# Performance work log

Hardware: AMD Instinct MI355X
Metric: run time of the kernel (lower is better)

Reference implementation:

```python
import jax, jax.numpy as jnp
import numpy as np

V = 256       # num_variables
D = 512       # hidden_dim
B = 1024      # batch


def setup_inputs() -> dict:
    key = jax.random.key(0)
    ks = jax.random.split(key, 8)
    s1 = 1.0 / np.sqrt(V + 1)
    s2 = 1.0 / np.sqrt(D)
    return {
        "x": jax.random.normal(ks[0], (B, V), dtype=jnp.float32),
        "adjacency": jax.random.normal(ks[1], (V, V), dtype=jnp.float32),
        "W1": jax.random.normal(ks[2], (V, D, V + 1), dtype=jnp.float32) * s1,
        "b1": jax.random.normal(ks[3], (V, D), dtype=jnp.float32) * s1,
        "W2": jax.random.normal(ks[4], (V, D, D), dtype=jnp.float32) * s2,
        "b2": jax.random.normal(ks[5], (V, D), dtype=jnp.float32) * s2,
        "W3": jax.random.normal(ks[6], (V, D), dtype=jnp.float32) * s2,
        "b3": jax.random.normal(ks[7], (V,), dtype=jnp.float32) * s2,
    }


def reference(x, adjacency, W1, b1, W2, b2, W3, b3):
    # weighted_x[b, i] = (x @ A.T)[b, i]
    wx = x @ adjacency.T  # [B, V]
    # combined input for variable i: cat([x, wx[:, i:i+1]]) -> width V+1
    # build [B, V, V+1] by broadcasting x across the variable axis
    x_b = jnp.broadcast_to(x[:, None, :], (x.shape[0], V, V))
    comb = jnp.concatenate([x_b, wx[:, :, None]], axis=-1)  # [B, V, V+1]
    # per-variable 3-layer MLP, batched over the variable axis i
    h1 = jax.nn.relu(jnp.einsum('bij,idj->bid', comb, W1) + b1)   # [B, V, D]
    h2 = jax.nn.relu(jnp.einsum('bid,ied->bie', h1, W2) + b2)     # [B, V, D]
    out = jnp.einsum('bid,id->bi', h2, W3) + b3                   # [B, V]
    return out
```

## Files before the change

kernel.cpp:

```cpp
#include <hip/hip_runtime.h>
#include <hip/hip_bf16.h>
#include <stdint.h>

#define VNUM 256
#define DNUM 512
#define BNUM 1024

typedef __attribute__((ext_vector_type(8))) short bf16x8;
typedef __attribute__((ext_vector_type(4))) float f32x4;

__device__ __forceinline__ uint16_t f2bf(float f) {
    uint32_t u = __float_as_uint(f);
    uint32_t r = (u + 0x7FFFu + ((u >> 16) & 1u)) >> 16;
    return (uint16_t)r;
}

__device__ __forceinline__ void gl_lds16(const void* g, void* l) {
    __builtin_amdgcn_global_load_lds(
        (const __attribute__((address_space(1))) uint32_t*)g,
        (__attribute__((address_space(3))) uint32_t*)l, 16, 0, 0);
}

__global__ __launch_bounds__(256) void wx_kernel(const float* __restrict__ x,
                                                 const float* __restrict__ adj,
                                                 float* __restrict__ wx) {
    __shared__ float xs[64][36];
    __shared__ float as_[64][36];
    const int b0 = blockIdx.x * 64, i0 = blockIdx.y * 64;
    const int t = threadIdx.x;
    const int tx = t & 15, ty = t >> 4;
    const int lr = t >> 2, lk = (t & 3) * 8;
    float c[4][4] = {};
    for (int k0 = 0; k0 < 256; k0 += 32) {
        __syncthreads();
        *(float4*)&xs[lr][lk]      = *(const float4*)&x[(size_t)(b0 + lr) * VNUM + k0 + lk];
        *(float4*)&xs[lr][lk + 4]  = *(const float4*)&x[(size_t)(b0 + lr) * VNUM + k0 + lk + 4];
        *(float4*)&as_[lr][lk]     = *(const float4*)&adj[(size_t)(i0 + lr) * VNUM + k0 + lk];
        *(float4*)&as_[lr][lk + 4] = *(const float4*)&adj[(size_t)(i0 + lr) * VNUM + k0 + lk + 4];
        __syncthreads();
        #pragma unroll
        for (int kk = 0; kk < 32; kk++) {
            float xv[4], av[4];
            #pragma unroll
            for (int a = 0; a < 4; a++) xv[a] = xs[ty + a * 16][kk];
            #pragma unroll
            for (int b = 0; b < 4; b++) av[b] = as_[tx + b * 16][kk];
            #pragma unroll
            for (int a = 0; a < 4; a++)
                #pragma unroll
                for (int b = 0; b < 4; b++) c[a][b] += xv[a] * av[b];
        }
    }
    #pragma unroll
    for (int a = 0; a < 4; a++)
        #pragma unroll
        for (int b = 0; b < 4; b++)
            wx[(size_t)(b0 + ty + a * 16) * VNUM + i0 + tx + b * 16] = c[a][b];
}

__global__ __launch_bounds__(256) void xcvt_kernel(const float* __restrict__ x,
                                                   uint16_t* __restrict__ xbf) {
    const int idx = (blockIdx.x * 256 + threadIdx.x) * 4;
    float4 v = *(const float4*)&x[idx];
    uint32_t p0 = (uint32_t)f2bf(v.x) | ((uint32_t)f2bf(v.y) << 16);
    uint32_t p1 = (uint32_t)f2bf(v.z) | ((uint32_t)f2bf(v.w) << 16);
    *(uint2*)&xbf[idx] = make_uint2(p0, p1);
}

__global__ __launch_bounds__(256) void gemm1_kernel(const uint16_t* __restrict__ xbf,
                                                    const float* __restrict__ wx,
                                                    const float* __restrict__ W1,
                                                    const float* __restrict__ b1,
                                                    uint16_t* __restrict__ h1,
                                                    int ivar_base) {
    const int b0 = blockIdx.x * 128;
    const int d0 = blockIdx.y * 128;
    const int ci = blockIdx.z;
    const int i  = ivar_base + ci;

    __shared__ __align__(16) uint16_t As[128 * 32];
    __shared__ __align__(16) uint16_t Bs[128 * 32];
    __shared__ float wxs[128], w1ls[128], b1s[128];

    const int t = threadIdx.x;
    const int w = t >> 6, l = t & 63;
    const int wm = w >> 1, wn = w & 1;
    const int q = l >> 4, lo = l & 15;

    if (t < 128) {
        wxs[t] = wx[(size_t)(b0 + t) * VNUM + i];
        b1s[t] = b1[(size_t)i * DNUM + d0 + t];
    } else {
        int tt = t - 128;
        w1ls[tt] = W1[((size_t)i * DNUM + d0 + tt) * 257 + 256];
    }

    f32x4 acc[4][4];
    #pragma unroll
    for (int a = 0; a < 4; a++)
        #pragma unroll
        for (int b = 0; b < 4; b++) { f32x4 z = {0.f, 0.f, 0.f, 0.f}; acc[a][b] = z; }

    const int br = t >> 1, kh = t & 1;
    const float* bsrc_row = W1 + ((size_t)i * DNUM + d0 + br) * 257 + kh * 16;
    const int sB = (br >> 1) & 3;
    const int bslot0 = br * 32 + (((kh * 2 + 0) ^ sB) * 8);
    const int bslot1 = br * 32 + (((kh * 2 + 1) ^ sB) * 8);

    for (int k0 = 0; k0 < 256; k0 += 32) {
        __syncthreads();
        #pragma unroll
        for (int p = 0; p < 2; p++) {
            int c  = p * 256 + w * 64 + l;
            int r  = c >> 2, k2 = c & 3;
            int gk2 = k2 ^ ((r >> 1) & 3);
            gl_lds16(xbf + (size_t)(b0 + r) * VNUM + k0 + gk2 * 8,
                     &As[(p * 256 + w * 64) * 8]);
        }
        {
            const float* s = bsrc_row + k0;
            float f[16];
            #pragma unroll
            for (int j = 0; j < 16; j++) f[j] = s[j];
            uint32_t pk[8];
            #pragma unroll
            for (int j = 0; j < 8; j++)
                pk[j] = (uint32_t)f2bf(f[2 * j]) | ((uint32_t)f2bf(f[2 * j + 1]) << 16);
            *(uint4*)&Bs[bslot0] = make_uint4(pk[0], pk[1], pk[2], pk[3]);
            *(uint4*)&Bs[bslot1] = make_uint4(pk[4], pk[5], pk[6], pk[7]);
        }
        __syncthreads();
        bf16x8 af[4], bfr[4];
        #pragma unroll
        for (int mt = 0; mt < 4; mt++) {
            int m = wm * 64 + mt * 16 + lo;
            int slot = q ^ ((m >> 1) & 3);
            af[mt] = *(const bf16x8*)&As[m * 32 + slot * 8];
        }
        #pragma unroll
        for (int nt = 0; nt < 4; nt++) {
            int n = wn * 64 + nt * 16 + lo;
            int slot = q ^ ((n >> 1) & 3);
            bfr[nt] = *(const bf16x8*)&Bs[n * 32 + slot * 8];
        }
        #pragma unroll
        for (int mt = 0; mt < 4; mt++)
            #pragma unroll
            for (int nt = 0; nt < 4; nt++)
                acc[mt][nt] = __builtin_amdgcn_mfma_f32_16x16x32_bf16(af[mt], bfr[nt], acc[mt][nt], 0, 0, 0);
    }

    #pragma unroll
    for (int mt = 0; mt < 4; mt++) {
        #pragma unroll
        for (int reg = 0; reg < 4; reg++) {
            int row = wm * 64 + mt * 16 + q * 4 + reg;
            size_t rowbase = ((size_t)ci * BNUM + b0 + row) * DNUM + d0;
            float wxv = wxs[row];
            #pragma unroll
            for (int nt = 0; nt < 4; nt++) {
                int col = wn * 64 + nt * 16 + lo;
                float v = acc[mt][nt][reg] + wxv * w1ls[col] + b1s[col];
                v = fmaxf(v, 0.f);
                h1[rowbase + col] = f2bf(v);
            }
        }
    }
}

__global__ __launch_bounds__(256) void gemm2_kernel(const uint16_t* __restrict__ h1,
                                                    const float* __restrict__ W2,
                                                    const float* __restrict__ b2,
                                                    const float* __restrict__ W3,
                                                    const float* __restrict__ b3,
                                                    float* __restrict__ out,
                                                    int ivar_base) {
    const int b0 = blockIdx.x * 128;
    const int e0 = blockIdx.y * 128;
    const int ci = blockIdx.z;
    const int i  = ivar_base + ci;

    __shared__ __align__(16) uint16_t As[128 * 32];
    __shared__ __align__(16) uint16_t Bs[128 * 32];
    __shared__ float b2s[128], w3s[128];
    __shared__ float red[2][128];

    const int t = threadIdx.x;
    const int w = t >> 6, l = t & 63;
    const int wm = w >> 1, wn = w & 1;
    const int q = l >> 4, lo = l & 15;

    if (t < 128) b2s[t] = b2[(size_t)i * DNUM + e0 + t];
    else         w3s[t - 128] = W3[(size_t)i * DNUM + e0 + (t - 128)];

    f32x4 acc[4][4];
    #pragma unroll
    for (int a = 0; a < 4; a++)
        #pragma unroll
        for (int b = 0; b < 4; b++) { f32x4 z = {0.f, 0.f, 0.f, 0.f}; acc[a][b] = z; }

    const int br = t >> 1, kh = t & 1;
    const float* bsrc_row = W2 + ((size_t)i * DNUM + e0 + br) * DNUM + kh * 16;
    const int sB = (br >> 1) & 3;
    const int bslot0 = br * 32 + (((kh * 2 + 0) ^ sB) * 8);
    const int bslot1 = br * 32 + (((kh * 2 + 1) ^ sB) * 8);

    const uint16_t* abase = h1 + (size_t)ci * BNUM * DNUM;

    for (int k0 = 0; k0 < 512; k0 += 32) {
        __syncthreads();
        #pragma unroll
        for (int p = 0; p < 2; p++) {
            int c  = p * 256 + w * 64 + l;
            int r  = c >> 2, k2 = c & 3;
            int gk2 = k2 ^ ((r >> 1) & 3);
            gl_lds16(abase + (size_t)(b0 + r) * DNUM + k0 + gk2 * 8,
                     &As[(p * 256 + w * 64) * 8]);
        }
        {
            const float4* s = (const float4*)(bsrc_row + k0);
            float4 fa = s[0], fb = s[1], fc = s[2], fd = s[3];
            uint32_t p0 = (uint32_t)f2bf(fa.x) | ((uint32_t)f2bf(fa.y) << 16);
            uint32_t p1 = (uint32_t)f2bf(fa.z) | ((uint32_t)f2bf(fa.w) << 16);
            uint32_t p2 = (uint32_t)f2bf(fb.x) | ((uint32_t)f2bf(fb.y) << 16);
            uint32_t p3 = (uint32_t)f2bf(fb.z) | ((uint32_t)f2bf(fb.w) << 16);
            uint32_t p4 = (uint32_t)f2bf(fc.x) | ((uint32_t)f2bf(fc.y) << 16);
            uint32_t p5 = (uint32_t)f2bf(fc.z) | ((uint32_t)f2bf(fc.w) << 16);
            uint32_t p6 = (uint32_t)f2bf(fd.x) | ((uint32_t)f2bf(fd.y) << 16);
            uint32_t p7 = (uint32_t)f2bf(fd.z) | ((uint32_t)f2bf(fd.w) << 16);
            *(uint4*)&Bs[bslot0] = make_uint4(p0, p1, p2, p3);
            *(uint4*)&Bs[bslot1] = make_uint4(p4, p5, p6, p7);
        }
        __syncthreads();
        bf16x8 af[4], bfr[4];
        #pragma unroll
        for (int mt = 0; mt < 4; mt++) {
            int m = wm * 64 + mt * 16 + lo;
            int slot = q ^ ((m >> 1) & 3);
            af[mt] = *(const bf16x8*)&As[m * 32 + slot * 8];
        }
        #pragma unroll
        for (int nt = 0; nt < 4; nt++) {
            int n = wn * 64 + nt * 16 + lo;
            int slot = q ^ ((n >> 1) & 3);
            bfr[nt] = *(const bf16x8*)&Bs[n * 32 + slot * 8];
        }
        #pragma unroll
        for (int mt = 0; mt < 4; mt++)
            #pragma unroll
            for (int nt = 0; nt < 4; nt++)
                acc[mt][nt] = __builtin_amdgcn_mfma_f32_16x16x32_bf16(af[mt], bfr[nt], acc[mt][nt], 0, 0, 0);
    }

    float rs[4][4];
    #pragma unroll
    for (int mt = 0; mt < 4; mt++) {
        #pragma unroll
        for (int reg = 0; reg < 4; reg++) {
            float v = 0.f;
            #pragma unroll
            for (int nt = 0; nt < 4; nt++) {
                int col = wn * 64 + nt * 16 + lo;
                float h = acc[mt][nt][reg] + b2s[col];
                h = fmaxf(h, 0.f);
                v += h * w3s[col];
            }
            v += __shfl_xor(v, 1, 64);
            v += __shfl_xor(v, 2, 64);
            v += __shfl_xor(v, 4, 64);
            v += __shfl_xor(v, 8, 64);
            rs[mt][reg] = v;
        }
    }
    if (lo == 0) {
        #pragma unroll
        for (int mt = 0; mt < 4; mt++)
            #pragma unroll
            for (int reg = 0; reg < 4; reg++) {
                int row = wm * 64 + mt * 16 + q * 4 + reg;
                red[wn][row] = rs[mt][reg];
            }
    }
    __syncthreads();
    if (t < 128) {
        float v = red[0][t] + red[1][t];
        if (e0 == 0) v += b3[i];
        atomicAdd(&out[(size_t)(b0 + t) * VNUM + i], v);
    }
}

extern "C" void kernel_launch(void* const* d_in, const int* in_sizes, int n_in,
                              void* d_out, int out_size, void* d_ws, size_t ws_size,
                              hipStream_t stream) {
    const float* x   = (const float*)d_in[0];
    const float* adj = (const float*)d_in[1];
    const float* W1  = (const float*)d_in[2];
    const float* b1  = (const float*)d_in[3];
    const float* W2  = (const float*)d_in[4];
    const float* b2  = (const float*)d_in[5];
    const float* W3  = (const float*)d_in[6];
    const float* b3  = (const float*)d_in[7];
    float* out = (float*)d_out;

    char* ws = (char*)d_ws;
    float*    wx  = (float*)ws;
    uint16_t* xbf = (uint16_t*)(ws + (1 << 20));
    uint16_t* h1  = (uint16_t*)(ws + (1 << 20) + (1 << 19));

    const size_t fixed = (1 << 20) + (1 << 19);
    int CV = 64;
    while (CV > 1 && ws_size < fixed + (size_t)CV * BNUM * DNUM * 2) CV >>= 1;

    hipMemsetAsync(d_out, 0, (size_t)BNUM * VNUM * sizeof(float), stream);
    wx_kernel<<<dim3(16, 4), 256, 0, stream>>>(x, adj, wx);
    xcvt_kernel<<<256, 256, 0, stream>>>(x, xbf);
    for (int c = 0; c < VNUM; c += CV) {
        gemm1_kernel<<<dim3(8, 4, CV), 256, 0, stream>>>(xbf, wx, W1, b1, h1, c);
        gemm2_kernel<<<dim3(8, 4, CV), 256, 0, stream>>>(h1, W2, b2, W3, b3, out, c);
    }
}
```

Measured before the change: 1.007 ms.

## Pre-convert W1/W2 to bf16 and run all variables in one launch

Adds separate kernels that convert W1 (splitting off its last column) and W2 to bf16 up front, so both GEMMs stream B tiles straight into LDS with global_load_lds instead of loading fp32, converting and storing per tile. It also drops the chunked loop over variables and launches each GEMM once over all 256 variables, which needs h1 for every variable in the workspace (about 256 MB). The cost is an extra full fp32 read plus bf16 write of the weights each call, in exchange for halving the weight bytes each GEMM tile reads and removing conversion work from the inner loop. It assumes the workspace is large enough and no longer checks ws_size.

```diff
diff --git a/kernel.cpp b/kernel.cpp
--- a/kernel.cpp
+++ b/kernel.cpp
@@ -67,16 +67,36 @@
     *(uint2*)&xbf[idx] = make_uint2(p0, p1);
 }
 
+__global__ __launch_bounds__(256) void w1cvt_kernel(const float* __restrict__ W1,
+                                                    uint16_t* __restrict__ W1bf,
+                                                    float* __restrict__ w1last) {
+    const size_t idx = (size_t)blockIdx.x * 256 + threadIdx.x;
+    const size_t row = idx >> 8;
+    const int    k   = (int)(idx & 255);
+    const float* src = W1 + row * 257;
+    W1bf[idx] = f2bf(src[k]);
+    if (k == 0) w1last[row] = src[256];
+}
+
+__global__ __launch_bounds__(256) void w2cvt_kernel(const float* __restrict__ W2,
+                                                    uint16_t* __restrict__ W2bf) {
+    const size_t idx = ((size_t)blockIdx.x * 256 + threadIdx.x) * 4;
+    float4 v = *(const float4*)&W2[idx];
+    uint32_t p0 = (uint32_t)f2bf(v.x) | ((uint32_t)f2bf(v.y) << 16);
+    uint32_t p1 = (uint32_t)f2bf(v.z) | ((uint32_t)f2bf(v.w) << 16);
+    *(uint2*)&W2bf[idx] = make_uint2(p0, p1);
+}
+
 __global__ __launch_bounds__(256) void gemm1_kernel(const uint16_t* __restrict__ xbf,
                                                     const float* __restrict__ wx,
-                                                    const float* __restrict__ W1,
+                                                    const uint16_t* __restrict__ W1bf,
+                                                    const float* __restrict__ w1last,
                                                     const float* __restrict__ b1,
-                                                    uint16_t* __restrict__ h1,
-                                                    int ivar_base) {
+                                                    uint16_t* __restrict__ h1) {
     const int b0 = blockIdx.x * 128;
     const int d0 = blockIdx.y * 128;
     const int ci = blockIdx.z;
-    const int i  = ivar_base + ci;
+    const int i  = ci;
 
     __shared__ __align__(16) uint16_t As[128 * 32];
     __shared__ __align__(16) uint16_t Bs[128 * 32];
@@ -92,7 +112,7 @@
         b1s[t] = b1[(size_t)i * DNUM + d0 + t];
     } else {
         int tt = t - 128;
-        w1ls[tt] = W1[((size_t)i * DNUM + d0 + tt) * 257 + 256];
+        w1ls[tt] = w1last[(size_t)i * DNUM + d0 + tt];
     }
 
     f32x4 acc[4][4];
@@ -101,11 +121,11 @@
         #pragma unroll
         for (int b = 0; b < 4; b++) { f32x4 z = {0.f, 0.f, 0.f, 0.f}; acc[a][b] = z; }
 
-    const int br = t >> 1, kh = t & 1;
-    const float* bsrc_row = W1 + ((size_t)i * DNUM + d0 + br) * 257 + kh * 16;
-    const int sB = (br >> 1) & 3;
-    const int bslot0 = br * 32 + (((kh * 2 + 0) ^ sB) * 8);
-    const int bslot1 = br * 32 + (((kh * 2 + 1) ^ sB) * 8);
+    const int c_  = w * 64 + l;
+    const int rA  = c_ >> 2,        kA = (c_ & 3) ^ ((rA >> 2) & 0);
+
+    const uint16_t* Abase = xbf;
+    const uint16_t* Bbase = W1bf + (size_t)i * DNUM * 256;
 
     for (int k0 = 0; k0 < 256; k0 += 32) {
         __syncthreads();
@@ -114,20 +134,16 @@
             int c  = p * 256 + w * 64 + l;
             int r  = c >> 2, k2 = c & 3;
             int gk2 = k2 ^ ((r >> 1) & 3);
-            gl_lds16(xbf + (size_t)(b0 + r) * VNUM + k0 + gk2 * 8,
+            gl_lds16(Abase + (size_t)(b0 + r) * 256 + k0 + gk2 * 8,
                      &As[(p * 256 + w * 64) * 8]);
         }
-        {
-            const float* s = bsrc_row + k0;
-            float f[16];
-            #pragma unroll
-            for (int j = 0; j < 16; j++) f[j] = s[j];
-            uint32_t pk[8];
-            #pragma unroll
-            for (int j = 0; j < 8; j++)
-                pk[j] = (uint32_t)f2bf(f[2 * j]) | ((uint32_t)f2bf(f[2 * j + 1]) << 16);
-            *(uint4*)&Bs[bslot0] = make_uint4(pk[0], pk[1], pk[2], pk[3]);
-            *(uint4*)&Bs[bslot1] = make_uint4(pk[4], pk[5], pk[6], pk[7]);
+        #pragma unroll
+        for (int p = 0; p < 2; p++) {
+            int c  = p * 256 + w * 64 + l;
+            int r  = c >> 2, k2 = c & 3;
+            int gk2 = k2 ^ ((r >> 1) & 3);
+            gl_lds16(Bbase + (size_t)(d0 + r) * 256 + k0 + gk2 * 8,
+                     &Bs[(p * 256 + w * 64) * 8]);
         }
         __syncthreads();
         bf16x8 af[4], bfr[4];
@@ -149,6 +165,7 @@
             for (int nt = 0; nt < 4; nt++)
                 acc[mt][nt] = __builtin_amdgcn_mfma_f32_16x16x32_bf16(af[mt], bfr[nt], acc[mt][nt], 0, 0, 0);
     }
+    (void)rA; (void)kA;
 
     #pragma unroll
     for (int mt = 0; mt < 4; mt++) {
@@ -169,16 +186,15 @@
 }
 
 __global__ __launch_bounds__(256) void gemm2_kernel(const uint16_t* __restrict__ h1,
-                                                    const float* __restrict__ W2,
+                                                    const uint16_t* __restrict__ W2bf,
                                                     const float* __restrict__ b2,
                                                     const float* __restrict__ W3,
                                                     const float* __restrict__ b3,
-                                                    float* __restrict__ out,
-                                                    int ivar_base) {
+                                                    float* __restrict__ out) {
     const int b0 = blockIdx.x * 128;
     const int e0 = blockIdx.y * 128;
     const int ci = blockIdx.z;
-    const int i  = ivar_base + ci;
+    const int i  = ci;
 
     __shared__ __align__(16) uint16_t As[128 * 32];
     __shared__ __align__(16) uint16_t Bs[128 * 32];
@@ -199,13 +215,8 @@
         #pragma unroll
         for (int b = 0; b < 4; b++) { f32x4 z = {0.f, 0.f, 0.f, 0.f}; acc[a][b] = z; }
 
-    const int br = t >> 1, kh = t & 1;
-    const float* bsrc_row = W2 + ((size_t)i * DNUM + e0 + br) * DNUM + kh * 16;
-    const int sB = (br >> 1) & 3;
-    const int bslot0 = br * 32 + (((kh * 2 + 0) ^ sB) * 8);
-    const int bslot1 = br * 32 + (((kh * 2 + 1) ^ sB) * 8);
-
-    const uint16_t* abase = h1 + (size_t)ci * BNUM * DNUM;
+    const uint16_t* Abase = h1 + (size_t)ci * BNUM * DNUM;
+    const uint16_t* Bbase = W2bf + (size_t)i * DNUM * DNUM;
 
     for (int k0 = 0; k0 < 512; k0 += 32) {
         __syncthreads();
@@ -214,22 +225,16 @@
             int c  = p * 256 + w * 64 + l;
             int r  = c >> 2, k2 = c & 3;
             int gk2 = k2 ^ ((r >> 1) & 3);
-            gl_lds16(abase + (size_t)(b0 + r) * DNUM + k0 + gk2 * 8,
+            gl_lds16(Abase + (size_t)(b0 + r) * DNUM + k0 + gk2 * 8,
                      &As[(p * 256 + w * 64) * 8]);
         }
-        {
-            const float4* s = (const float4*)(bsrc_row + k0);
-            float4 fa = s[0], fb = s[1], fc = s[2], fd = s[3];
-            uint32_t p0 = (uint32_t)f2bf(fa.x) | ((uint32_t)f2bf(fa.y) << 16);
-            uint32_t p1 = (uint32_t)f2bf(fa.z) | ((uint32_t)f2bf(fa.w) << 16);
-            uint32_t p2 = (uint32_t)f2bf(fb.x) | ((uint32_t)f2bf(fb.y) << 16);
-            uint32_t p3 = (uint32_t)f2bf(fb.z) | ((uint32_t)f2bf(fb.w) << 16);
-            uint32_t p4 = (uint32_t)f2bf(fc.x) | ((uint32_t)f2bf(fc.y) << 16);
-            uint32_t p5 = (uint32_t)f2bf(fc.z) | ((uint32_t)f2bf(fc.w) << 16);
-            uint32_t p6 = (uint32_t)f2bf(fd.x) | ((uint32_t)f2bf(fd.y) << 16);
-            uint32_t p7 = (uint32_t)f2bf(fd.z) | ((uint32_t)f2bf(fd.w) << 16);
-            *(uint4*)&Bs[bslot0] = make_uint4(p0, p1, p2, p3);
-            *(uint4*)&Bs[bslot1] = make_uint4(p4, p5, p6, p7);
+        #pragma unroll
+        for (int p = 0; p < 2; p++) {
+            int c  = p * 256 + w * 64 + l;
+            int r  = c >> 2, k2 = c & 3;
+            int gk2 = k2 ^ ((r >> 1) & 3);
+            gl_lds16(Bbase + (size_t)(e0 + r) * DNUM + k0 + gk2 * 8,
+                     &Bs[(p * 256 + w * 64) * 8]);
         }
         __syncthreads();
         bf16x8 af[4], bfr[4];
@@ -303,19 +308,21 @@
     float* out = (float*)d_out;
 
     char* ws = (char*)d_ws;
-    float*    wx  = (float*)ws;
-    uint16_t* xbf = (uint16_t*)(ws + (1 << 20));
-    uint16_t* h1  = (uint16_t*)(ws + (1 << 20) + (1 << 19));
-
-    const size_t fixed = (1 << 20) + (1 << 19);
-    int CV = 64;
-    while (CV > 1 && ws_size < fixed + (size_t)CV * BNUM * DNUM * 2) CV >>= 1;
+    float*    wx     = (float*)ws;
+    uint16_t* xbf    = (uint16_t*)(ws + (1 << 20));
+    float*    w1last = (float*)(ws + (1 << 20) + (1 << 19));
+    char*     p      = ws + (2 << 20);
+    uint16_t* W1bf   = (uint16_t*)p;
+    p += (size_t)VNUM * DNUM * 256 * 2;
+    uint16_t* W2bf   = (uint16_t*)p;
+    p += (size_t)VNUM * DNUM * DNUM * 2;
+    uint16_t* h1     = (uint16_t*)p;
 
     hipMemsetAsync(d_out, 0, (size_t)BNUM * VNUM * sizeof(float), stream);
     wx_kernel<<<dim3(16, 4), 256, 0, stream>>>(x, adj, wx);
     xcvt_kernel<<<256, 256, 0, stream>>>(x, xbf);
-    for (int c = 0; c < VNUM; c += CV) {
-        gemm1_kernel<<<dim3(8, 4, CV), 256, 0, stream>>>(xbf, wx, W1, b1, h1, c);
-        gemm2_kernel<<<dim3(8, 4, CV), 256, 0, stream>>>(h1, W2, b2, W3, b3, out, c);
-    }
-}
+    w1cvt_kernel<<<(VNUM * DNUM * 256) / 256, 256, 0, stream>>>(W1, W1bf, w1last);
+    w2cvt_kernel<<<(VNUM * DNUM * DNUM) / (4 * 256), 256, 0, stream>>>(W2, W2bf);
+    gemm1_kernel<<<dim3(8, 4, VNUM), 256, 0, stream>>>(xbf, wx, W1bf, w1last, b1, h1);
+    gemm2_kernel<<<dim3(8, 4, VNUM), 256, 0, stream>>>(h1, W2bf, b2, W3, b3, out);
+}
```

Measured after the change: 891.3 us. 1.13x faster.
